# Kernel tuning notes

Measured on AMD Instinct MI355X. Metric: run time of the kernel, lower is better.

The kernel has to match this reference:

```python
import jax, jax.numpy as jnp
import numpy as np

B = 4096
ED = 128          # EMBEDDING_DIM
HD = 64           # HIDDEN_DIM
LH = 128          # LSTM_HIDDEN_DIM
IN_DIM = ED * (12 + 48 + 1)  # 7808
N_ABILITY, N_MOVE = 300, 900


def setup_inputs() -> dict:
    key = jax.random.key(0)
    ks = jax.random.split(key, 16)
    s = lambda k, shape, scale=0.05: (jax.random.normal(k, shape, dtype=jnp.float32) * scale)
    return {
        "ability_ids": jax.random.randint(ks[0], (B, 12), 0, N_ABILITY),
        "move_ids": jax.random.randint(ks[1], (B, 48), 0, N_MOVE),
        "numerical": s(ks[2], (B, 84), 1.0),
        "mask": (jax.random.uniform(ks[3], (B, 9)) > 0.3).astype(jnp.float32),
        "h0": jnp.zeros((B, LH), jnp.float32),
        "c0": jnp.zeros((B, LH), jnp.float32),
        "ability_emb": s(ks[4], (N_ABILITY, ED), 1.0),
        "move_emb": s(ks[5], (N_MOVE, ED), 1.0),
        "num_W": s(ks[6], (ED, 84)),
        "num_b": s(ks[7], (ED,)),
        "Wih": s(ks[8], (4 * LH, IN_DIM), 0.01),
        "Whh": s(ks[9], (4 * LH, LH)),
        "bih": s(ks[10], (4 * LH,)),
        "bhh": s(ks[11], (4 * LH,)),
        "W1": s(ks[12], (HD, LH)),
        "b1": s(ks[13], (HD,)),
        "W2": s(ks[14], (ED, HD)),
        "b2": s(ks[15], (ED,)),
        "Wa": s(jax.random.fold_in(key, 100), (9, ED)),
        "ba": s(jax.random.fold_in(key, 101), (9,)),
    }


def reference(ability_ids, move_ids, numerical, mask, h0, c0,
              ability_emb, move_emb, num_W, num_b,
              Wih, Whh, bih, bhh, W1, b1, W2, b2, Wa, ba):
    # Gather + concat: [B, 12*ED] + [B, 48*ED] + [B, ED] -> [B, 7808]
    ab = ability_emb[ability_ids].reshape(ability_ids.shape[0], 12 * ED)
    mv = move_emb[move_ids].reshape(move_ids.shape[0], 48 * ED)
    num = numerical @ num_W.T + num_b
    x = jnp.concatenate([ab, mv, num], axis=-1)

    # Single-timestep LSTM (torch gate order: i, f, g, o)
    gates = x @ Wih.T + bih + h0 @ Whh.T + bhh
    i, f, g, o = jnp.split(gates, 4, axis=-1)
    i, f, o = jax.nn.sigmoid(i), jax.nn.sigmoid(f), jax.nn.sigmoid(o)
    g = jnp.tanh(g)
    c1 = f * c0 + i * g
    h1 = o * jnp.tanh(c1)

    # MLP head + action logits
    feat = jax.nn.relu(h1 @ W1.T + b1) @ W2.T + b2
    probs = jax.nn.softmax(feat @ Wa.T + ba, axis=-1)

    # Masked renormalization; fall back to unmasked probs when mask kills everything
    masked = probs * mask
    ssum = masked.sum(-1, keepdims=True)
    out = jnp.where(ssum > 0, masked / jnp.where(ssum > 0, ssum, 1.0), probs)
    return out, h1, c1
```

## Files before the change

kernel.cpp:

```cpp
#include <hip/hip_runtime.h>
#include <hip/hip_bf16.h>
#include <stdint.h>
#include <stddef.h>

typedef __bf16 bf16;
typedef __bf16 bf16x4 __attribute__((ext_vector_type(4)));
typedef __bf16 bf16x8 __attribute__((ext_vector_type(8)));
typedef float f32x4 __attribute__((ext_vector_type(4)));

#define BATCH 4096
#define KIH 7808
#define KTOT 7936
#define NG 512
#define LH 128
#define HD 64
#define ED 128
#define SPLITK 4

#define OFF_WCAT 0u
#define OFF_GPART 8126464u
#define OFF_XT   24903680u
#define OFF_AB   27000832u
#define OFF_MV   27077632u
#define OFF_ADDR 27308032u
#define OFF_H1B  28356608u
#define OFF_W1F  29405184u
#define OFF_W2F  29421568u
#define OFF_WAF  29437952u
#define OFF_NB   29442048u

#define O_H1 (BATCH * 9)
#define O_C1 (BATCH * 9 + BATCH * LH)

#define PREP_BP 2048
#define PREP_CW (PREP_BP + 512)
#define PREP_CE (PREP_CW + 150)
#define PREP_TOT (PREP_CE + 1)

typedef const __attribute__((address_space(1))) uint32_t* gas_ptr;
typedef __attribute__((address_space(3))) uint32_t* las_ptr;

__device__ __forceinline__ void async16(const void* g, void* l) {
    __builtin_amdgcn_global_load_lds((gas_ptr)g, (las_ptr)l, 16, 0, 0);
}

__global__ void prep(const int* __restrict__ ab_ids,
                     const int* __restrict__ mv_ids,
                     const float* __restrict__ numerical,
                     const float* __restrict__ h0,
                     const float* __restrict__ numW,
                     const float* __restrict__ numb,
                     const float* __restrict__ Wih,
                     const float* __restrict__ Whh,
                     const float* __restrict__ ab_emb,
                     const float* __restrict__ mv_emb,
                     const float* __restrict__ W1,
                     const float* __restrict__ W2,
                     const float* __restrict__ Wa,
                     uint8_t* __restrict__ ws) {
    const int bid = blockIdx.x;
    const int t = threadIdx.x;

    if (bid < PREP_BP) {
        bf16* xtail = (bf16*)(ws + OFF_XT);
        uint32_t* addrs = (uint32_t*)(ws + OFF_ADDR);
        const int h = t >> 7;
        const int th = t & 127;
        const int b = bid * 2 + h;

        __shared__ int ids[2][60];
        if (th < 60)
            ids[h][th] = (th < 12) ? ab_ids[b * 12 + th]
                                   : mv_ids[b * 48 + (th - 12)];

        const float v = (th < 84) ? numerical[(size_t)b * 84 + th] : 0.f;
        xtail[(size_t)b * 256 + th] = (bf16)v;
        xtail[(size_t)b * 256 + 128 + th] = (bf16)h0[(size_t)b * LH + th];
        __syncthreads();

        if (th < 64) {
            uint32_t off;
            if (th < 12) off = OFF_AB + (uint32_t)ids[h][th] * 256u;
            else if (th < 60) off = OFF_MV + (uint32_t)ids[h][th] * 256u;
            else if (th == 60) off = OFF_XT + (uint32_t)b * 512u;
            else if (th == 61) off = OFF_XT + (uint32_t)b * 512u + 256u;
            else off = OFF_XT;
            addrs[(size_t)b * 64 + th] = off;
        }
    } else if (bid < PREP_CW) {
        bf16* Wcat = (bf16*)(ws + OFF_WCAT);
        float* nbias = (float*)(ws + OFF_NB);
        const int n = bid - PREP_BP;

        __shared__ float wrow[128];
        __shared__ float nbs[128];
        if (t < 128) wrow[t] = Wih[(size_t)n * KIH + 7680 + t];
        else nbs[t - 128] = numb[t - 128];
        __syncthreads();

        const float* src_ih = Wih + (size_t)n * KIH;
        bf16* dst = Wcat + (size_t)n * KTOT;
        for (int k4 = t; k4 < 1920; k4 += 256) {
            const int k = k4 * 4;
            const float4 v = *(const float4*)(src_ih + k);
            bf16x4 o = {(bf16)v.x, (bf16)v.y, (bf16)v.z, (bf16)v.w};
            *(bf16x4*)(dst + k) = o;
        }
        if (t < 84) {
            float acc = 0.f;
#pragma unroll 4
            for (int e = 0; e < 128; ++e)
                acc += wrow[e] * numW[e * 84 + t];
            dst[7680 + t] = (bf16)acc;
        } else if (t < 128) {
            dst[7680 + t] = (bf16)0.f;
        } else {
            const int tt = t - 128;
            dst[KIH + tt] = (bf16)Whh[(size_t)n * LH + tt];
        }
        if (t == 255) {
            float a = 0.f;
#pragma unroll 4
            for (int e = 0; e < 128; ++e) a += wrow[e] * nbs[e];
            nbias[n] = a;
        }
    } else if (bid < PREP_CE) {
        bf16* ab8 = (bf16*)(ws + OFF_AB);
        bf16* mv8 = (bf16*)(ws + OFF_MV);
        const int i = ((bid - PREP_CW) * 256 + t) * 4;
        const bool isab = i < 300 * 128;
        const float4 v = isab ? *(const float4*)(ab_emb + i)
                              : *(const float4*)(mv_emb + (i - 300 * 128));
        bf16x4 o = {(bf16)v.x, (bf16)v.y, (bf16)v.z, (bf16)v.w};
        if (isab) *(bf16x4*)(ab8 + i) = o;
        else *(bf16x4*)(mv8 + (i - 300 * 128)) = o;
    } else {
        bf16* W1f = (bf16*)(ws + OFF_W1F);
        bf16* W2f = (bf16*)(ws + OFF_W2F);
        bf16* Waf = (bf16*)(ws + OFF_WAF);
        for (int e = t; e < 8192; e += 256) {
            const int j = e & 7, ln = (e >> 3) & 63, fid = e >> 9;
            const int kt = fid & 3, nt = fid >> 2;
            const int n = nt * 16 + (ln & 15);
            const int k = kt * 32 + (ln >> 4) * 8 + j;
            W1f[e] = (bf16)W1[n * 128 + k];
        }
        for (int e = t; e < 8192; e += 256) {
            const int j = e & 7, ln = (e >> 3) & 63, fid = e >> 9;
            const int kt = fid & 1, nt = fid >> 1;
            const int n = nt * 16 + (ln & 15);
            const int k = kt * 32 + (ln >> 4) * 8 + j;
            W2f[e] = (bf16)W2[n * 64 + k];
        }
        for (int e = t; e < 2048; e += 256) {
            const int j = e & 7, ln = (e >> 3) & 63, kt = e >> 9;
            const int n = ln & 15;
            const int k = kt * 32 + (ln >> 4) * 8 + j;
            Waf[e] = (n < 9) ? (bf16)Wa[n * 128 + k] : (bf16)0.f;
        }
    }
}

__global__ __launch_bounds__(256, 2) void gemm_gates(
    const uint8_t* __restrict__ wsbase,
    const bf16* __restrict__ Wcat,
    const uint32_t* __restrict__ addrs,
    bf16* __restrict__ gpart) {
    __shared__ bf16 As[2][128 * 64];
    __shared__ bf16 Bs[2][128 * 64];
    __shared__ uint32_t adr[17][128];

    const int tid = threadIdx.x;
    const int w = tid >> 6;
    const int lane = tid & 63;
    const int bm = blockIdx.x;
    const int bn = blockIdx.y;
    const int bz = blockIdx.z;
    const int kt_beg = bz * 31;
    const int kt_end = kt_beg + 31;

    const int s0 = kt_beg >> 1;
    const int ns = ((kt_end - 1) >> 1) - s0 + 1;
    for (int i = tid; i < ns * 128; i += 256) {
        adr[i >> 7][i & 127] =
            addrs[(size_t)(bm * 128 + (i & 127)) * 64 + s0 + (i >> 7)];
    }

    const int r_l = lane >> 3;
    const int sc16 = ((lane & 7) ^ r_l) * 16;

    const int wn = w & 1;
    const int wk = w >> 1;
    const int n0 = wn * 64;
    const int kk8 = wk * 4 + (lane >> 4);
    const int fl = lane & 15;

    f32x4 acc[8][4];
#pragma unroll
    for (int i = 0; i < 8; ++i)
#pragma unroll
        for (int j = 0; j < 4; ++j)
#pragma unroll
            for (int r = 0; r < 4; ++r) acc[i][j][r] = 0.f;

    __syncthreads();

    auto stage = [&](int kt, int pb) {
        const int k0 = kt * 64;
        const int sl = (kt >> 1) - s0;
        const int hb = (kt & 1) * 128;
#pragma unroll
        for (int j = 0; j < 4; ++j) {
            const int row = (w * 4 + j) * 8 + r_l;
            const uint8_t* gsrc = wsbase + adr[sl][row] + hb + sc16;
            async16(gsrc, (void*)&As[pb][((w * 4 + j) * 64 + lane) * 8]);
        }
#pragma unroll
        for (int j = 0; j < 4; ++j) {
            const int row = (w * 4 + j) * 8 + r_l;
            const bf16* gsrc = Wcat + (size_t)(bn * 128 + row) * KTOT + k0 + (sc16 >> 1);
            async16(gsrc, (void*)&Bs[pb][((w * 4 + j) * 64 + lane) * 8]);
        }
    };

    stage(kt_beg, 0);

    for (int kt = kt_beg; kt < kt_end; ++kt) {
        const int pb = (kt - kt_beg) & 1;
        __syncthreads();
        if (kt + 1 < kt_end) stage(kt + 1, pb ^ 1);

        const bf16* Ab = &As[pb][0];
        const bf16* Bb = &Bs[pb][0];

        bf16x8 bfr[4];
#pragma unroll
        for (int tj = 0; tj < 4; ++tj) {
            const int n = n0 + tj * 16 + fl;
            bfr[tj] = *(const bf16x8*)&Bb[n * 64 + ((kk8 ^ (n & 7)) * 8)];
        }
#pragma unroll
        for (int ti = 0; ti < 8; ++ti) {
            const int m = ti * 16 + fl;
            const bf16x8 af = *(const bf16x8*)&Ab[m * 64 + ((kk8 ^ (m & 7)) * 8)];
#pragma unroll
            for (int tj = 0; tj < 4; ++tj)
                acc[ti][tj] = __builtin_amdgcn_mfma_f32_16x16x32_bf16(
                    af, bfr[tj], acc[ti][tj], 0, 0, 0);
        }
    }

    __syncthreads();
    float* red = (wn == 0) ? (float*)&As[0][0] : (float*)&Bs[0][0];
    if (wk == 1) {
#pragma unroll
        for (int ti = 0; ti < 8; ++ti)
#pragma unroll
            for (int tj = 0; tj < 4; ++tj)
#pragma unroll
                for (int r = 0; r < 4; ++r)
                    red[((ti * 4 + tj) * 4 + r) * 64 + lane] = acc[ti][tj][r];
    }
    __syncthreads();

    if (wk == 0) {
        bf16* gdst = gpart + (size_t)bz * BATCH * NG;
        const int mlo = (lane >> 4) * 4;
#pragma unroll
        for (int ti = 0; ti < 8; ++ti)
#pragma unroll
            for (int tj = 0; tj < 4; ++tj) {
                const int mg = bm * 128 + ti * 16 + mlo;
                const int ng = bn * 128 + n0 + tj * 16 + fl;
                bf16* dst = gdst + (size_t)mg * NG + ng;
#pragma unroll
                for (int r = 0; r < 4; ++r)
                    dst[(size_t)r * NG] = (bf16)(
                        acc[ti][tj][r] + red[((ti * 4 + tj) * 4 + r) * 64 + lane]);
            }
    }
}

__global__ void reduce_lstm(const bf16* __restrict__ gpart,
                            const float* __restrict__ bih,
                            const float* __restrict__ bhh,
                            const float* __restrict__ nbias,
                            const float* __restrict__ c0,
                            float* __restrict__ out,
                            bf16* __restrict__ h1b) {
    const int t = threadIdx.x;
    const int b = blockIdx.x * 2 + (t >> 7);
    const int u = t & 127;

    float gv[4];
#pragma unroll
    for (int q = 0; q < 4; ++q)
        gv[q] = bih[q * 128 + u] + bhh[q * 128 + u] + nbias[q * 128 + u];
#pragma unroll
    for (int z = 0; z < SPLITK; ++z) {
        const bf16* gz = gpart + ((size_t)z * BATCH + b) * NG + u;
#pragma unroll
        for (int q = 0; q < 4; ++q) gv[q] += (float)gz[q * 128];
    }

    const float iv = 1.f / (1.f + __expf(-gv[0]));
    const float fv = 1.f / (1.f + __expf(-gv[1]));
    const float gg = tanhf(gv[2]);
    const float ov = 1.f / (1.f + __expf(-gv[3]));
    const float c1 = fv * c0[(size_t)b * LH + u] + iv * gg;
    const float h1 = ov * tanhf(c1);

    out[O_H1 + (size_t)b * LH + u] = h1;
    out[O_C1 + (size_t)b * LH + u] = c1;
    h1b[(size_t)b * LH + u] = (bf16)h1;
}

__global__ __launch_bounds__(64) void mlp_head(
    const bf16* __restrict__ h1b, const float* __restrict__ mask,
    const bf16* __restrict__ W1f, const bf16* __restrict__ W2f,
    const bf16* __restrict__ Waf,
    const float* __restrict__ b1, const float* __restrict__ b2,
    const float* __restrict__ ba,
    float* __restrict__ out) {
    __shared__ bf16 uS[16 * 64];
    __shared__ bf16 fS[16 * 128];

    const int lane = threadIdx.x;
    const int b0 = blockIdx.x * 16;
    const int nl = lane & 15, kg = lane >> 4;

    bf16x8 ah[4];
#pragma unroll
    for (int kt = 0; kt < 4; ++kt)
        ah[kt] = *(const bf16x8*)&h1b[(size_t)(b0 + nl) * 128 + kt * 32 + kg * 8];

#pragma unroll
    for (int nt = 0; nt < 4; ++nt) {
        f32x4 a = {0.f, 0.f, 0.f, 0.f};
#pragma unroll
        for (int kt = 0; kt < 4; ++kt)
            a = __builtin_amdgcn_mfma_f32_16x16x32_bf16(
                ah[kt], *(const bf16x8*)&W1f[((nt * 4 + kt) * 64 + lane) * 8],
                a, 0, 0, 0);
        const int n = nt * 16 + nl;
        const float bb = b1[n];
#pragma unroll
        for (int r = 0; r < 4; ++r)
            uS[(kg * 4 + r) * 64 + n] = (bf16)fmaxf(a[r] + bb, 0.f);
    }
    __syncthreads();

    bf16x8 au[2];
#pragma unroll
    for (int kt = 0; kt < 2; ++kt)
        au[kt] = *(const bf16x8*)&uS[nl * 64 + kt * 32 + kg * 8];

#pragma unroll
    for (int nt = 0; nt < 8; ++nt) {
        f32x4 a = {0.f, 0.f, 0.f, 0.f};
#pragma unroll
        for (int kt = 0; kt < 2; ++kt)
            a = __builtin_amdgcn_mfma_f32_16x16x32_bf16(
                au[kt], *(const bf16x8*)&W2f[((nt * 2 + kt) * 64 + lane) * 8],
                a, 0, 0, 0);
        const int n = nt * 16 + nl;
        const float bb = b2[n];
#pragma unroll
        for (int r = 0; r < 4; ++r)
            fS[(kg * 4 + r) * 128 + n] = (bf16)(a[r] + bb);
    }
    __syncthreads();

    bf16x8 afr[4];
#pragma unroll
    for (int kt = 0; kt < 4; ++kt)
        afr[kt] = *(const bf16x8*)&fS[nl * 128 + kt * 32 + kg * 8];

    f32x4 lg4 = {0.f, 0.f, 0.f, 0.f};
#pragma unroll
    for (int kt = 0; kt < 4; ++kt)
        lg4 = __builtin_amdgcn_mfma_f32_16x16x32_bf16(
            afr[kt], *(const bf16x8*)&Waf[(kt * 64 + lane) * 8], lg4, 0, 0, 0);

    const float bav = (nl < 9) ? ba[nl] : 0.f;

#pragma unroll
    for (int r = 0; r < 4; ++r) {
        const int b = b0 + kg * 4 + r;
        float lg = (nl < 9) ? lg4[r] + bav : -1e30f;
        float mx = lg;
#pragma unroll
        for (int off = 1; off < 16; off <<= 1)
            mx = fmaxf(mx, __shfl_xor(mx, off, 64));
        const float e = (nl < 9) ? __expf(lg - mx) : 0.f;
        const float mv = (nl < 9) ? mask[(size_t)b * 9 + nl] : 0.f;
        float tot = e, ms = e * mv;
#pragma unroll
        for (int off = 1; off < 16; off <<= 1) {
            tot += __shfl_xor(tot, off, 64);
            ms += __shfl_xor(ms, off, 64);
        }
        if (nl < 9)
            out[(size_t)b * 9 + nl] = (ms > 0.f) ? e * mv / ms : e / tot;
    }
}

extern "C" void kernel_launch(void* const* d_in, const int* in_sizes, int n_in,
                              void* d_out, int out_size, void* d_ws, size_t ws_size,
                              hipStream_t stream) {
    const int* ab_ids = (const int*)d_in[0];
    const int* mv_ids = (const int*)d_in[1];
    const float* numerical = (const float*)d_in[2];
    const float* mask = (const float*)d_in[3];
    const float* h0 = (const float*)d_in[4];
    const float* c0 = (const float*)d_in[5];
    const float* ab_emb = (const float*)d_in[6];
    const float* mv_emb = (const float*)d_in[7];
    const float* numW = (const float*)d_in[8];
    const float* numb = (const float*)d_in[9];
    const float* Wih = (const float*)d_in[10];
    const float* Whh = (const float*)d_in[11];
    const float* bih = (const float*)d_in[12];
    const float* bhh = (const float*)d_in[13];
    const float* W1 = (const float*)d_in[14];
    const float* b1 = (const float*)d_in[15];
    const float* W2 = (const float*)d_in[16];
    const float* b2 = (const float*)d_in[17];
    const float* Wa = (const float*)d_in[18];
    const float* ba = (const float*)d_in[19];
    float* out = (float*)d_out;

    uint8_t* ws = (uint8_t*)d_ws;
    bf16* Wcat = (bf16*)(ws + OFF_WCAT);
    bf16* gpart = (bf16*)(ws + OFF_GPART);
    uint32_t* addrs = (uint32_t*)(ws + OFF_ADDR);
    bf16* h1b = (bf16*)(ws + OFF_H1B);
    bf16* W1f = (bf16*)(ws + OFF_W1F);
    bf16* W2f = (bf16*)(ws + OFF_W2F);
    bf16* Waf = (bf16*)(ws + OFF_WAF);
    float* nbias = (float*)(ws + OFF_NB);

    prep<<<PREP_TOT, 256, 0, stream>>>(
        ab_ids, mv_ids, numerical, h0, numW, numb, Wih, Whh, ab_emb, mv_emb,
        W1, W2, Wa, ws);
    gemm_gates<<<dim3(32, 4, SPLITK), 256, 0, stream>>>(ws, Wcat, addrs, gpart);
    reduce_lstm<<<BATCH / 2, 256, 0, stream>>>(gpart, bih, bhh, nbias, c0,
                                               out, h1b);
    mlp_head<<<BATCH / 16, 64, 0, stream>>>(h1b, mask, W1f, W2f, Waf,
                                            b1, b2, ba, out);
}
```

Measured before the change: 167.4 us.

## Pre-swizzle gate weights into MFMA fragment layout and load B directly to registers

The prep kernel now writes the concatenated LSTM weight matrix in an MFMA-fragment-ordered layout, so each lane's bf16x8 B operand is one contiguous 16-byte global load. The GEMM drops the B shared-memory buffer and its async staging and loads B fragments straight from global into registers, issued before staging the next A tile. The split-K reduction between warp pairs is done in two halves to fit in the smaller shared memory. This halves LDS use and LDS traffic per block, which may raise occupancy, but B loads are no longer prefetched a stage ahead, so global latency may be exposed and B tiles are no longer shared through LDS across the block.

```diff
diff --git a/kernel.cpp b/kernel.cpp
--- a/kernel.cpp
+++ b/kernel.cpp
@@ -36,6 +36,14 @@
 #define PREP_CW (PREP_BP + 512)
 #define PREP_CE (PREP_CW + 150)
 #define PREP_TOT (PREP_CE + 1)
+
+__device__ __forceinline__ size_t wcatf_idx(int n, int k) {
+    const int ntile = n >> 4;
+    const int lane = (n & 15) + (((k >> 3) & 3) << 4);
+    const int kc = k >> 5;
+    const int j = k & 7;
+    return ((((size_t)ntile * 248 + kc) << 6) + lane) * 8 + j;
+}
 
 typedef const __attribute__((address_space(1))) uint32_t* gas_ptr;
 typedef __attribute__((address_space(3))) uint32_t* las_ptr;
@@ -88,7 +96,7 @@
             addrs[(size_t)b * 64 + th] = off;
         }
     } else if (bid < PREP_CW) {
-        bf16* Wcat = (bf16*)(ws + OFF_WCAT);
+        bf16* WcatF = (bf16*)(ws + OFF_WCAT);
         float* nbias = (float*)(ws + OFF_NB);
         const int n = bid - PREP_BP;
 
@@ -99,24 +107,23 @@
         __syncthreads();
 
         const float* src_ih = Wih + (size_t)n * KIH;
-        bf16* dst = Wcat + (size_t)n * KTOT;
         for (int k4 = t; k4 < 1920; k4 += 256) {
             const int k = k4 * 4;
             const float4 v = *(const float4*)(src_ih + k);
             bf16x4 o = {(bf16)v.x, (bf16)v.y, (bf16)v.z, (bf16)v.w};
-            *(bf16x4*)(dst + k) = o;
+            *(bf16x4*)&WcatF[wcatf_idx(n, k)] = o;
         }
         if (t < 84) {
             float acc = 0.f;
 #pragma unroll 4
             for (int e = 0; e < 128; ++e)
                 acc += wrow[e] * numW[e * 84 + t];
-            dst[7680 + t] = (bf16)acc;
+            WcatF[wcatf_idx(n, 7680 + t)] = (bf16)acc;
         } else if (t < 128) {
-            dst[7680 + t] = (bf16)0.f;
+            WcatF[wcatf_idx(n, 7680 + t)] = (bf16)0.f;
         } else {
             const int tt = t - 128;
-            dst[KIH + tt] = (bf16)Whh[(size_t)n * LH + tt];
+            WcatF[wcatf_idx(n, KIH + tt)] = (bf16)Whh[(size_t)n * LH + tt];
         }
         if (t == 255) {
             float a = 0.f;
@@ -163,11 +170,10 @@
 
 __global__ __launch_bounds__(256, 2) void gemm_gates(
     const uint8_t* __restrict__ wsbase,
-    const bf16* __restrict__ Wcat,
+    const bf16* __restrict__ WcatF,
     const uint32_t* __restrict__ addrs,
     bf16* __restrict__ gpart) {
     __shared__ bf16 As[2][128 * 64];
-    __shared__ bf16 Bs[2][128 * 64];
     __shared__ uint32_t adr[17][128];
 
     const int tid = threadIdx.x;
@@ -206,7 +212,6 @@
     __syncthreads();
 
     auto stage = [&](int kt, int pb) {
-        const int k0 = kt * 64;
         const int sl = (kt >> 1) - s0;
         const int hb = (kt & 1) * 128;
 #pragma unroll
@@ -215,12 +220,6 @@
             const uint8_t* gsrc = wsbase + adr[sl][row] + hb + sc16;
             async16(gsrc, (void*)&As[pb][((w * 4 + j) * 64 + lane) * 8]);
         }
-#pragma unroll
-        for (int j = 0; j < 4; ++j) {
-            const int row = (w * 4 + j) * 8 + r_l;
-            const bf16* gsrc = Wcat + (size_t)(bn * 128 + row) * KTOT + k0 + (sc16 >> 1);
-            async16(gsrc, (void*)&Bs[pb][((w * 4 + j) * 64 + lane) * 8]);
-        }
     };
 
     stage(kt_beg, 0);
@@ -228,17 +227,17 @@
     for (int kt = kt_beg; kt < kt_end; ++kt) {
         const int pb = (kt - kt_beg) & 1;
         __syncthreads();
+
+        const int kc = kt * 2 + wk;
+        bf16x8 bfr[4];
+#pragma unroll
+        for (int tj = 0; tj < 4; ++tj)
+            bfr[tj] = *(const bf16x8*)&WcatF[
+                ((((size_t)(bn * 8 + wn * 4 + tj) * 248 + kc) << 6) + lane) * 8];
+
         if (kt + 1 < kt_end) stage(kt + 1, pb ^ 1);
 
         const bf16* Ab = &As[pb][0];
-        const bf16* Bb = &Bs[pb][0];
-
-        bf16x8 bfr[4];
-#pragma unroll
-        for (int tj = 0; tj < 4; ++tj) {
-            const int n = n0 + tj * 16 + fl;
-            bfr[tj] = *(const bf16x8*)&Bb[n * 64 + ((kk8 ^ (n & 7)) * 8)];
-        }
 #pragma unroll
         for (int ti = 0; ti < 8; ++ti) {
             const int m = ti * 16 + fl;
@@ -250,34 +249,38 @@
         }
     }
 
-    __syncthreads();
-    float* red = (wn == 0) ? (float*)&As[0][0] : (float*)&Bs[0][0];
-    if (wk == 1) {
-#pragma unroll
-        for (int ti = 0; ti < 8; ++ti)
-#pragma unroll
-            for (int tj = 0; tj < 4; ++tj)
-#pragma unroll
-                for (int r = 0; r < 4; ++r)
-                    red[((ti * 4 + tj) * 4 + r) * 64 + lane] = acc[ti][tj][r];
-    }
-    __syncthreads();
-
-    if (wk == 0) {
-        bf16* gdst = gpart + (size_t)bz * BATCH * NG;
-        const int mlo = (lane >> 4) * 4;
-#pragma unroll
-        for (int ti = 0; ti < 8; ++ti)
-#pragma unroll
-            for (int tj = 0; tj < 4; ++tj) {
-                const int mg = bm * 128 + ti * 16 + mlo;
-                const int ng = bn * 128 + n0 + tj * 16 + fl;
-                bf16* dst = gdst + (size_t)mg * NG + ng;
-#pragma unroll
-                for (int r = 0; r < 4; ++r)
-                    dst[(size_t)r * NG] = (bf16)(
-                        acc[ti][tj][r] + red[((ti * 4 + tj) * 4 + r) * 64 + lane]);
-            }
+    float* redf = (float*)&As[0][0];
+    bf16* gdst = gpart + (size_t)bz * BATCH * NG;
+    const int mlo = (lane >> 4) * 4;
+#pragma unroll
+    for (int h = 0; h < 2; ++h) {
+        __syncthreads();
+        if (wk == 1) {
+#pragma unroll
+            for (int ti = 0; ti < 4; ++ti)
+#pragma unroll
+                for (int tj = 0; tj < 4; ++tj)
+#pragma unroll
+                    for (int r = 0; r < 4; ++r)
+                        redf[wn * 4096 + ((ti * 4 + tj) * 4 + r) * 64 + lane] =
+                            acc[h * 4 + ti][tj][r];
+        }
+        __syncthreads();
+        if (wk == 0) {
+#pragma unroll
+            for (int ti = 0; ti < 4; ++ti)
+#pragma unroll
+                for (int tj = 0; tj < 4; ++tj) {
+                    const int mg = bm * 128 + (h * 4 + ti) * 16 + mlo;
+                    const int ng = bn * 128 + n0 + tj * 16 + fl;
+                    bf16* dst = gdst + (size_t)mg * NG + ng;
+#pragma unroll
+                    for (int r = 0; r < 4; ++r)
+                        dst[(size_t)r * NG] = (bf16)(
+                            acc[h * 4 + ti][tj][r] +
+                            redf[wn * 4096 + ((ti * 4 + tj) * 4 + r) * 64 + lane]);
+                }
+        }
     }
 }
 
@@ -431,7 +434,7 @@
     float* out = (float*)d_out;
 
     uint8_t* ws = (uint8_t*)d_ws;
-    bf16* Wcat = (bf16*)(ws + OFF_WCAT);
+    bf16* WcatF = (bf16*)(ws + OFF_WCAT);
     bf16* gpart = (bf16*)(ws + OFF_GPART);
     uint32_t* addrs = (uint32_t*)(ws + OFF_ADDR);
     bf16* h1b = (bf16*)(ws + OFF_H1B);
@@ -443,7 +446,7 @@
     prep<<<PREP_TOT, 256, 0, stream>>>(
         ab_ids, mv_ids, numerical, h0, numW, numb, Wih, Whh, ab_emb, mv_emb,
         W1, W2, Wa, ws);
-    gemm_gates<<<dim3(32, 4, SPLITK), 256, 0, stream>>>(ws, Wcat, addrs, gpart);
+    gemm_gates<<<dim3(32, 4, SPLITK), 256, 0, stream>>>(ws, WcatF, addrs, gpart);
     reduce_lstm<<<BATCH / 2, 256, 0, stream>>>(gpart, bih, bhh, nbias, c0,
                                                out, h1b);
     mlp_head<<<BATCH / 16, 64, 0, stream>>>(h1b, mask, W1f, W2f, Waf,
```

Result: no change. 168.1 us (+0.4%).
